# Performance work log

Hardware: AMD Instinct MI355X
Metric: run time of the kernel (lower is better)

Reference implementation:

```python
import jax, jax.numpy as jnp
import numpy as np

M, K, N = 4096, 4096, 4096

def setup_inputs() -> dict:
    key = jax.random.key(0)
    k1, k2, k3 = jax.random.split(key, 3)
    a = jax.random.randint(k1, (M, K), 0, 127, dtype=jnp.int32)
    b = jax.random.randint(k2, (K, N), 0, 127, dtype=jnp.int32)
    scale = jax.random.uniform(k3, (N,), dtype=jnp.float32)
    return {"a": a, "b": b, "scale": scale}

def reference(a, b, scale):
    a8 = a.astype(jnp.int8)
    b8 = b.astype(jnp.int8)
    acc = jnp.matmul(a8, b8, preferred_element_type=jnp.int32)  # [M, N] int32
    # fused per-column (per-output-channel) dequantization scale
    return acc.astype(jnp.float32) * scale[None, :]  # [M, N] float32
```

## Files before the change

### kernel.cpp

```cpp
#include <hip/hip_runtime.h>
#include <stdint.h>

#define M_DIM 4096
#define K_DIM 4096
#define N_DIM 4096

typedef int v4i __attribute__((ext_vector_type(4)));
typedef int int32x4 __attribute__((ext_vector_type(4)));

__device__ __forceinline__ void gload_lds16(const void* g, void* l) {
    __builtin_amdgcn_global_load_lds(
        (const __attribute__((address_space(1))) uint32_t*)g,
        (__attribute__((address_space(3))) uint32_t*)l, 16, 0, 0);
}

__global__ void pack_ab_kernel(const int* __restrict__ a, char* __restrict__ a8,
                               const int* __restrict__ b, char* __restrict__ b8t) {
    __shared__ char tile[64][68];
    if (blockIdx.x < 2048) {
        int idx = blockIdx.x * 256 + threadIdx.x;
        const int stride = 2048 * 256;
        const int total4 = M_DIM * K_DIM / 4;
        for (int i = idx; i < total4; i += stride) {
            int32x4 v = ((const int32x4*)a)[i];
            uint32_t p = (uint32_t)(v.x & 0xff) | ((uint32_t)(v.y & 0xff) << 8) |
                         ((uint32_t)(v.z & 0xff) << 16) | ((uint32_t)(v.w & 0xff) << 24);
            ((uint32_t*)a8)[i] = p;
        }
    } else {
        int bid2 = blockIdx.x - 2048;
        int n0 = (bid2 & 63) * 64;
        int k0 = (bid2 >> 6) * 64;
        int tx = threadIdx.x & 63;
        int ty = threadIdx.x >> 6;
#pragma unroll
        for (int kk = 0; kk < 64; kk += 4) {
            tile[kk + ty][tx] = (char)b[(size_t)(k0 + kk + ty) * N_DIM + n0 + tx];
        }
        __syncthreads();
        int td = threadIdx.x & 15;
        int tn = threadIdx.x >> 4;
#pragma unroll
        for (int nn0 = 0; nn0 < 64; nn0 += 16) {
            int nn = nn0 + tn;
            uint32_t p = (uint32_t)(uint8_t)tile[td * 4 + 0][nn] |
                         ((uint32_t)(uint8_t)tile[td * 4 + 1][nn] << 8) |
                         ((uint32_t)(uint8_t)tile[td * 4 + 2][nn] << 16) |
                         ((uint32_t)(uint8_t)tile[td * 4 + 3][nn] << 24);
            *(uint32_t*)&b8t[(size_t)(n0 + nn) * K_DIM + k0 + td * 4] = p;
        }
    }
}

#define BM 256
#define BN 256
#define BK 128
#define KTILES (K_DIM / BK)

#define BAR __builtin_amdgcn_s_barrier()
#define WAIT_VM4 asm volatile("s_waitcnt vmcnt(4)" ::: "memory")
#define WAIT_VM0 asm volatile("s_waitcnt vmcnt(0)" ::: "memory")

#define DS_A(dst, kk, ib)                                                               \
    _Pragma("unroll") for (int i_ = 0; i_ < 4; ++i_) dst[i_] =                          \
        *(const v4i*)(lds + bufOff + (kk) * 16384 + aOff + ((ib) + i_) * 1024);

#define DS_B(dst, kk)                                                                   \
    _Pragma("unroll") for (int j_ = 0; j_ < 4; ++j_) dst[j_] =                          \
        *(const v4i*)(lds + bufOff + (kk) * 16384 + bOff + j_ * 1024);

#define MM(ib, AF, BF)                                                                  \
    __builtin_amdgcn_s_setprio(1);                                                      \
    _Pragma("unroll") for (int i_ = 0; i_ < 4; ++i_)                                    \
    _Pragma("unroll") for (int j_ = 0; j_ < 4; ++j_)                                    \
        acc[(ib) + i_][j_] =                                                            \
            __builtin_amdgcn_mfma_i32_16x16x64_i8(AF[i_], BF[j_], acc[(ib) + i_][j_],   \
                                                  0, 0, 0);                             \
    __builtin_amdgcn_s_setprio(0);

__global__ __launch_bounds__(512, 2) void gemm_i8_slip(const char* __restrict__ A8,
                                                       const char* __restrict__ B8T,
                                                       const float* __restrict__ scale,
                                                       float* __restrict__ out) {
    __shared__ char lds[131072];

    int tid = threadIdx.x;
    int wave = tid >> 6;
    int lane = tid & 63;
    int wr = wave >> 2;
    int wc = wave & 3;
    int l15 = lane & 15;

    int bid = blockIdx.x;
    int swz = (bid & 7) * 32 + (bid >> 3);
    int bm = swz >> 4;
    int bn = swz & 15;

    int rA = tid >> 2;
    int cc = ((tid & 3) ^ ((tid >> 3) & 3)) << 4;
    const char* aSrc = A8 + (size_t)(bm * BM + rA) * K_DIM + cc;
    const char* bSrc = B8T + (size_t)(bn * BN + rA) * K_DIM + cc;

    int slot = (((lane >> 4) ^ ((lane >> 1) & 3)) << 4);
    int aOff = wr * 8192 + l15 * 64 + slot;
    int bOff = 32768 + wc * 4096 + l15 * 64 + slot;

    v4i acc[8][4];
#pragma unroll
    for (int i = 0; i < 8; ++i)
#pragma unroll
        for (int j = 0; j < 4; ++j) acc[i][j] = (v4i){0, 0, 0, 0};

    auto stage = [&](const char* srcBase, int kt1, int kk, int dstOff) {
        const char* s = srcBase + (size_t)kt1 * BK + kk * 64;
        char* d = (char*)lds + dstOff + wave * 1024;
        gload_lds16(s, d);
        gload_lds16(s + (size_t)128 * K_DIM, d + 8192);
    };

    stage(aSrc, 0, 0, 0);
    stage(bSrc, 0, 0, 32768);
    stage(aSrc, 0, 1, 16384);
    stage(bSrc, 0, 1, 49152);
    WAIT_VM4;
    BAR;

    int bufOff = 0;
    v4i a03[4], a47[4], b0[4];

    for (int kt = 0; kt < KTILES - 1; ++kt) {
        int nbufOff = bufOff ^ 65536;
        stage(aSrc, kt + 1, 0, nbufOff + 0);
        stage(bSrc, kt + 1, 0, nbufOff + 32768);
        DS_A(a03, 0, 0);
        DS_B(b0, 0);
        DS_A(a47, 0, 4);
        MM(0, a03, b0);
        MM(4, a47, b0);
        WAIT_VM4;
        BAR;
        stage(aSrc, kt + 1, 1, nbufOff + 16384);
        stage(bSrc, kt + 1, 1, nbufOff + 49152);
        DS_A(a03, 1, 0);
        DS_B(b0, 1);
        DS_A(a47, 1, 4);
        MM(0, a03, b0);
        MM(4, a47, b0);
        WAIT_VM4;
        BAR;
        bufOff = nbufOff;
    }

    DS_A(a03, 0, 0);
    DS_B(b0, 0);
    DS_A(a47, 0, 4);
    MM(0, a03, b0);
    MM(4, a47, b0);
    WAIT_VM0;
    BAR;
    DS_A(a03, 1, 0);
    DS_B(b0, 1);
    DS_A(a47, 1, 4);
    MM(0, a03, b0);
    MM(4, a47, b0);

    size_t orow0 = (size_t)bm * BM + wr * 128 + (lane >> 4) * 4;
    int ocol0 = bn * BN + wc * 64 + l15;
#pragma unroll
    for (int j = 0; j < 4; ++j) {
        int col = ocol0 + j * 16;
        float s = scale[col];
#pragma unroll
        for (int i = 0; i < 8; ++i) {
            size_t row = orow0 + (size_t)i * 16;
#pragma unroll
            for (int r = 0; r < 4; ++r) {
                out[(row + r) * N_DIM + col] = (float)acc[i][j][r] * s;
            }
        }
    }
}

#define FBM 128
#define FBN 128
#define FBK 64

__global__ __launch_bounds__(256) void gemm_i8_fused_kernel(const int* __restrict__ a,
                                                            const int* __restrict__ b,
                                                            const float* __restrict__ scale,
                                                            float* __restrict__ out) {
    __shared__ char As[FBM * FBK];
    __shared__ char Bs[FBN * FBK];

    int tid = threadIdx.x;
    int wave = tid >> 6;
    int lane = tid & 63;

    int nwg = gridDim.x;
    int cpx = nwg >> 3;
    int bid = blockIdx.x;
    int swz = (bid & 7) * cpx + (bid >> 3);
    int bm = swz >> 5;
    int bn = swz & 31;

    int f0 = tid * 16;
    int m0 = f0 >> 6;
    int k0 = f0 & 63;

    int nn = tid & 127;
    int kh = tid >> 7;

    int wr = wave >> 1;
    int wc = wave & 1;
    int lrow = lane & 15;
    int kgrp = (lane >> 4) * 16;

    v4i acc[4][4];
#pragma unroll
    for (int i = 0; i < 4; ++i)
#pragma unroll
        for (int j = 0; j < 4; ++j) acc[i][j] = (v4i){0, 0, 0, 0};

    const int kTiles = K_DIM / FBK;
    for (int kt = 0; kt < kTiles; ++kt) {
        __syncthreads();
#pragma unroll
        for (int r = 0; r < 2; ++r) {
            const int* src = a + (size_t)(bm * FBM + m0 + r * 64) * K_DIM + kt * FBK + k0;
            uint32_t pk[4];
#pragma unroll
            for (int q = 0; q < 4; ++q) {
                int32x4 v = *(const int32x4*)(src + q * 4);
                pk[q] = (uint32_t)(v.x & 0xff) | ((uint32_t)(v.y & 0xff) << 8) |
                        ((uint32_t)(v.z & 0xff) << 16) | ((uint32_t)(v.w & 0xff) << 24);
            }
            *(v4i*)&As[f0 + r * 4096] = (v4i){(int)pk[0], (int)pk[1], (int)pk[2], (int)pk[3]};
        }
#pragma unroll
        for (int d = 0; d < 8; ++d) {
            uint32_t p = 0;
#pragma unroll
            for (int i = 0; i < 4; ++i) {
                int kk = kt * FBK + kh * 32 + d * 4 + i;
                p |= (uint32_t)(b[(size_t)kk * N_DIM + bn * FBN + nn] & 0xff) << (8 * i);
            }
            *(uint32_t*)&Bs[nn * 64 + kh * 32 + d * 4] = p;
        }
        __syncthreads();

        v4i aF[4], bF[4];
#pragma unroll
        for (int i = 0; i < 4; ++i)
            aF[i] = *(const v4i*)&As[(wr * 64 + i * 16 + lrow) * FBK + kgrp];
#pragma unroll
        for (int j = 0; j < 4; ++j)
            bF[j] = *(const v4i*)&Bs[(wc * 64 + j * 16 + lrow) * FBK + kgrp];
#pragma unroll
        for (int i = 0; i < 4; ++i)
#pragma unroll
            for (int j = 0; j < 4; ++j)
                acc[i][j] = __builtin_amdgcn_mfma_i32_16x16x64_i8(aF[i], bF[j], acc[i][j], 0, 0, 0);
    }

    size_t orow0 = (size_t)bm * FBM + wr * 64;
    int ocol0 = bn * FBN + wc * 64;
#pragma unroll
    for (int j = 0; j < 4; ++j) {
        int col = ocol0 + j * 16 + lrow;
        float s = scale[col];
#pragma unroll
        for (int i = 0; i < 4; ++i) {
            size_t row = orow0 + i * 16 + (lane >> 4) * 4;
#pragma unroll
            for (int r = 0; r < 4; ++r) {
                out[(row + r) * N_DIM + col] = (float)acc[i][j][r] * s;
            }
        }
    }
}

extern "C" void kernel_launch(void* const* d_in, const int* in_sizes, int n_in,
                              void* d_out, int out_size, void* d_ws, size_t ws_size,
                              hipStream_t stream) {
    const int* a = (const int*)d_in[0];
    const int* b = (const int*)d_in[1];
    const float* scale = (const float*)d_in[2];
    float* out = (float*)d_out;

    size_t need = (size_t)M_DIM * K_DIM + (size_t)K_DIM * N_DIM;
    if (ws_size >= need) {
        char* a8 = (char*)d_ws;
        char* b8t = a8 + (size_t)M_DIM * K_DIM;
        pack_ab_kernel<<<2048 + 4096, 256, 0, stream>>>(a, a8, b, b8t);
        gemm_i8_slip<<<256, 512, 0, stream>>>(a8, b8t, scale, out);
    } else {
        gemm_i8_fused_kernel<<<1024, 256, 0, stream>>>(a, b, scale, out);
    }
}
```

Baseline: 97.44 us.

## Deepen GEMM LDS prefetch pipeline to three half-tile stages in flight

Restructures the K-loop so each half-tile's global-to-LDS load is issued one half-tile earlier, reusing the just-consumed half of the current buffer for tile kt+2. This keeps more global loads in flight (wait on vmcnt(8) instead of vmcnt(4)) to hide memory latency behind MFMA work. It adds a peeled epilogue for the last two tiles and relies on barrier ordering to avoid overwriting LDS that is still being read.

New measurement: 94.29 us. 1.03x faster.

```diff
diff --git a/kernel.cpp b/kernel.cpp
--- a/kernel.cpp
+++ b/kernel.cpp
@@ -58,16 +58,17 @@
 #define KTILES (K_DIM / BK)
 
 #define BAR __builtin_amdgcn_s_barrier()
+#define WAIT_VM8 asm volatile("s_waitcnt vmcnt(8)" ::: "memory")
 #define WAIT_VM4 asm volatile("s_waitcnt vmcnt(4)" ::: "memory")
 #define WAIT_VM0 asm volatile("s_waitcnt vmcnt(0)" ::: "memory")
 
-#define DS_A(dst, kk, ib)                                                               \
+#define DS_A(dst, bo, kk, ib)                                                           \
     _Pragma("unroll") for (int i_ = 0; i_ < 4; ++i_) dst[i_] =                          \
-        *(const v4i*)(lds + bufOff + (kk) * 16384 + aOff + ((ib) + i_) * 1024);
-
-#define DS_B(dst, kk)                                                                   \
+        *(const v4i*)(lds + (bo) + (kk) * 16384 + aOff + ((ib) + i_) * 1024);
+
+#define DS_B(dst, bo, kk)                                                               \
     _Pragma("unroll") for (int j_ = 0; j_ < 4; ++j_) dst[j_] =                          \
-        *(const v4i*)(lds + bufOff + (kk) * 16384 + bOff + j_ * 1024);
+        *(const v4i*)(lds + (bo) + (kk) * 16384 + bOff + j_ * 1024);
 
 #define MM(ib, AF, BF)                                                                  \
     __builtin_amdgcn_s_setprio(1);                                                      \
@@ -78,7 +79,7 @@
                                                   0, 0, 0);                             \
     __builtin_amdgcn_s_setprio(0);
 
-__global__ __launch_bounds__(512, 2) void gemm_i8_slip(const char* __restrict__ A8,
+__global__ __launch_bounds__(512, 2) void gemm_i8_deep(const char* __restrict__ A8,
                                                        const char* __restrict__ B8T,
                                                        const float* __restrict__ scale,
                                                        float* __restrict__ out) {
@@ -122,47 +123,68 @@
     stage(bSrc, 0, 0, 32768);
     stage(aSrc, 0, 1, 16384);
     stage(bSrc, 0, 1, 49152);
-    WAIT_VM4;
+    stage(aSrc, 1, 0, 65536 + 0);
+    stage(bSrc, 1, 0, 65536 + 32768);
+    WAIT_VM8;
     BAR;
 
-    int bufOff = 0;
     v4i a03[4], a47[4], b0[4];
 
-    for (int kt = 0; kt < KTILES - 1; ++kt) {
-        int nbufOff = bufOff ^ 65536;
-        stage(aSrc, kt + 1, 0, nbufOff + 0);
-        stage(bSrc, kt + 1, 0, nbufOff + 32768);
-        DS_A(a03, 0, 0);
-        DS_B(b0, 0);
-        DS_A(a47, 0, 4);
+    for (int kt = 0; kt < KTILES - 2; ++kt) {
+        int curBuf = (kt & 1) << 16;
+        int nxtBuf = curBuf ^ 65536;
+        stage(aSrc, kt + 1, 1, nxtBuf + 16384);
+        stage(bSrc, kt + 1, 1, nxtBuf + 49152);
+        DS_A(a03, curBuf, 0, 0);
+        DS_B(b0, curBuf, 0);
+        DS_A(a47, curBuf, 0, 4);
+        MM(0, a03, b0);
+        MM(4, a47, b0);
+        WAIT_VM8;
+        BAR;
+        stage(aSrc, kt + 2, 0, curBuf + 0);
+        stage(bSrc, kt + 2, 0, curBuf + 32768);
+        DS_A(a03, curBuf, 1, 0);
+        DS_B(b0, curBuf, 1);
+        DS_A(a47, curBuf, 1, 4);
+        MM(0, a03, b0);
+        MM(4, a47, b0);
+        WAIT_VM8;
+        BAR;
+    }
+
+    {
+        const int curBuf = ((KTILES - 2) & 1) << 16;
+        const int nxtBuf = curBuf ^ 65536;
+        stage(aSrc, KTILES - 1, 1, nxtBuf + 16384);
+        stage(bSrc, KTILES - 1, 1, nxtBuf + 49152);
+        DS_A(a03, curBuf, 0, 0);
+        DS_B(b0, curBuf, 0);
+        DS_A(a47, curBuf, 0, 4);
+        MM(0, a03, b0);
+        MM(4, a47, b0);
+        WAIT_VM8;
+        BAR;
+        DS_A(a03, curBuf, 1, 0);
+        DS_B(b0, curBuf, 1);
+        DS_A(a47, curBuf, 1, 4);
         MM(0, a03, b0);
         MM(4, a47, b0);
         WAIT_VM4;
         BAR;
-        stage(aSrc, kt + 1, 1, nbufOff + 16384);
-        stage(bSrc, kt + 1, 1, nbufOff + 49152);
-        DS_A(a03, 1, 0);
-        DS_B(b0, 1);
-        DS_A(a47, 1, 4);
-        MM(0, a03, b0);
-        MM(4, a47, b0);
-        WAIT_VM4;
-        BAR;
-        bufOff = nbufOff;
-    }
-
-    DS_A(a03, 0, 0);
-    DS_B(b0, 0);
-    DS_A(a47, 0, 4);
-    MM(0, a03, b0);
-    MM(4, a47, b0);
-    WAIT_VM0;
-    BAR;
-    DS_A(a03, 1, 0);
-    DS_B(b0, 1);
-    DS_A(a47, 1, 4);
-    MM(0, a03, b0);
-    MM(4, a47, b0);
+        DS_A(a03, nxtBuf, 0, 0);
+        DS_B(b0, nxtBuf, 0);
+        DS_A(a47, nxtBuf, 0, 4);
+        MM(0, a03, b0);
+        MM(4, a47, b0);
+        WAIT_VM0;
+        BAR;
+        DS_A(a03, nxtBuf, 1, 0);
+        DS_B(b0, nxtBuf, 1);
+        DS_A(a47, nxtBuf, 1, 4);
+        MM(0, a03, b0);
+        MM(4, a47, b0);
+    }
 
     size_t orow0 = (size_t)bm * BM + wr * 128 + (lane >> 4) * 4;
     int ocol0 = bn * BN + wc * 64 + l15;
@@ -292,7 +314,7 @@
         char* a8 = (char*)d_ws;
         char* b8t = a8 + (size_t)M_DIM * K_DIM;
         pack_ab_kernel<<<2048 + 4096, 256, 0, stream>>>(a, a8, b, b8t);
-        gemm_i8_slip<<<256, 512, 0, stream>>>(a8, b8t, scale, out);
+        gemm_i8_deep<<<256, 512, 0, stream>>>(a8, b8t, scale, out);
     } else {
         gemm_i8_fused_kernel<<<1024, 256, 0, stream>>>(a, b, scale, out);
     }
```

## Replace 256x256 int8 GEMM with smaller 128x128 tiles and higher occupancy

Applied to the files above, without the earlier changes.

Swaps the large-tile GEMM (256x256x128, 512 threads, 128KB LDS, 2 waves/SIMD pairs) for a 128x128x64 tile kernel with 256 threads, 32KB LDS and 4 blocks per CU, launched over 1024 blocks. The pipeline becomes a simple two-deep double buffer with one MFMA group per k-step. The goal is to rely on thread-level parallelism to hide latency instead of the intra-wave software pipeline. In exchange, reuse per loaded byte is halved, so global and LDS traffic per MFMA rise.

Result: slower. 120.1 us (+23.3%).

```diff
diff --git a/kernel.cpp b/kernel.cpp
--- a/kernel.cpp
+++ b/kernel.cpp
@@ -52,49 +52,40 @@
     }
 }
 
-#define BM 256
-#define BN 256
-#define BK 128
+#define BM 128
+#define BN 128
+#define BK 64
 #define KTILES (K_DIM / BK)
 
 #define BAR __builtin_amdgcn_s_barrier()
 #define WAIT_VM4 asm volatile("s_waitcnt vmcnt(4)" ::: "memory")
 #define WAIT_VM0 asm volatile("s_waitcnt vmcnt(0)" ::: "memory")
 
-#define DS_A(dst, kk, ib)                                                               \
-    _Pragma("unroll") for (int i_ = 0; i_ < 4; ++i_) dst[i_] =                          \
-        *(const v4i*)(lds + bufOff + (kk) * 16384 + aOff + ((ib) + i_) * 1024);
-
-#define DS_B(dst, kk)                                                                   \
-    _Pragma("unroll") for (int j_ = 0; j_ < 4; ++j_) dst[j_] =                          \
-        *(const v4i*)(lds + bufOff + (kk) * 16384 + bOff + j_ * 1024);
-
-#define MM(ib, AF, BF)                                                                  \
+#define MM16(AF, BF)                                                                    \
     __builtin_amdgcn_s_setprio(1);                                                      \
     _Pragma("unroll") for (int i_ = 0; i_ < 4; ++i_)                                    \
     _Pragma("unroll") for (int j_ = 0; j_ < 4; ++j_)                                    \
-        acc[(ib) + i_][j_] =                                                            \
-            __builtin_amdgcn_mfma_i32_16x16x64_i8(AF[i_], BF[j_], acc[(ib) + i_][j_],   \
-                                                  0, 0, 0);                             \
+        acc[i_][j_] =                                                                   \
+            __builtin_amdgcn_mfma_i32_16x16x64_i8(AF[i_], BF[j_], acc[i_][j_], 0, 0, 0);\
     __builtin_amdgcn_s_setprio(0);
 
-__global__ __launch_bounds__(512, 2) void gemm_i8_slip(const char* __restrict__ A8,
-                                                       const char* __restrict__ B8T,
-                                                       const float* __restrict__ scale,
-                                                       float* __restrict__ out) {
-    __shared__ char lds[131072];
+__global__ __launch_bounds__(256, 4) void gemm_i8_tlp(const char* __restrict__ A8,
+                                                      const char* __restrict__ B8T,
+                                                      const float* __restrict__ scale,
+                                                      float* __restrict__ out) {
+    __shared__ char lds[32768];
 
     int tid = threadIdx.x;
     int wave = tid >> 6;
     int lane = tid & 63;
-    int wr = wave >> 2;
-    int wc = wave & 3;
+    int wr = wave >> 1;
+    int wc = wave & 1;
     int l15 = lane & 15;
 
     int bid = blockIdx.x;
-    int swz = (bid & 7) * 32 + (bid >> 3);
-    int bm = swz >> 4;
-    int bn = swz & 15;
+    int swz = (bid & 7) * 128 + (bid >> 3);
+    int bm = swz >> 5;
+    int bn = swz & 31;
 
     int rA = tid >> 2;
     int cc = ((tid & 3) ^ ((tid >> 3) & 3)) << 4;
@@ -102,76 +93,71 @@
     const char* bSrc = B8T + (size_t)(bn * BN + rA) * K_DIM + cc;
 
     int slot = (((lane >> 4) ^ ((lane >> 1) & 3)) << 4);
-    int aOff = wr * 8192 + l15 * 64 + slot;
-    int bOff = 32768 + wc * 4096 + l15 * 64 + slot;
-
-    v4i acc[8][4];
-#pragma unroll
-    for (int i = 0; i < 8; ++i)
+    int aOff = wr * 4096 + l15 * 64 + slot;
+    int bOff = 8192 + wc * 4096 + l15 * 64 + slot;
+
+    v4i acc[4][4];
+#pragma unroll
+    for (int i = 0; i < 4; ++i)
 #pragma unroll
         for (int j = 0; j < 4; ++j) acc[i][j] = (v4i){0, 0, 0, 0};
 
-    auto stage = [&](const char* srcBase, int kt1, int kk, int dstOff) {
-        const char* s = srcBase + (size_t)kt1 * BK + kk * 64;
-        char* d = (char*)lds + dstOff + wave * 1024;
-        gload_lds16(s, d);
-        gload_lds16(s + (size_t)128 * K_DIM, d + 8192);
+    auto stage = [&](int kt, int bo) {
+        const char* sa = aSrc + (size_t)kt * BK;
+        const char* sb = bSrc + (size_t)kt * BK;
+        char* da = (char*)lds + bo + wave * 1024;
+        char* db = da + 8192;
+        gload_lds16(sa, da);
+        gload_lds16(sa + (size_t)64 * K_DIM, da + 4096);
+        gload_lds16(sb, db);
+        gload_lds16(sb + (size_t)64 * K_DIM, db + 4096);
     };
 
-    stage(aSrc, 0, 0, 0);
-    stage(bSrc, 0, 0, 32768);
-    stage(aSrc, 0, 1, 16384);
-    stage(bSrc, 0, 1, 49152);
+    stage(0, 0);
+    stage(1, 16384);
     WAIT_VM4;
     BAR;
 
-    int bufOff = 0;
-    v4i a03[4], a47[4], b0[4];
-
-    for (int kt = 0; kt < KTILES - 1; ++kt) {
-        int nbufOff = bufOff ^ 65536;
-        stage(aSrc, kt + 1, 0, nbufOff + 0);
-        stage(bSrc, kt + 1, 0, nbufOff + 32768);
-        DS_A(a03, 0, 0);
-        DS_B(b0, 0);
-        DS_A(a47, 0, 4);
-        MM(0, a03, b0);
-        MM(4, a47, b0);
+    v4i aF[4], bF[4];
+
+    for (int kt = 0; kt < KTILES - 2; ++kt) {
+        int cur = (kt & 1) << 14;
+#pragma unroll
+        for (int i = 0; i < 4; ++i) aF[i] = *(const v4i*)(lds + cur + aOff + i * 1024);
+#pragma unroll
+        for (int j = 0; j < 4; ++j) bF[j] = *(const v4i*)(lds + cur + bOff + j * 1024);
+        MM16(aF, bF);
+        BAR;
+        stage(kt + 2, cur);
         WAIT_VM4;
         BAR;
-        stage(aSrc, kt + 1, 1, nbufOff + 16384);
-        stage(bSrc, kt + 1, 1, nbufOff + 49152);
-        DS_A(a03, 1, 0);
-        DS_B(b0, 1);
-        DS_A(a47, 1, 4);
-        MM(0, a03, b0);
-        MM(4, a47, b0);
-        WAIT_VM4;
+    }
+
+    {
+        int cur = ((KTILES - 2) & 1) << 14;
+#pragma unroll
+        for (int i = 0; i < 4; ++i) aF[i] = *(const v4i*)(lds + cur + aOff + i * 1024);
+#pragma unroll
+        for (int j = 0; j < 4; ++j) bF[j] = *(const v4i*)(lds + cur + bOff + j * 1024);
+        MM16(aF, bF);
+        WAIT_VM0;
         BAR;
-        bufOff = nbufOff;
-    }
-
-    DS_A(a03, 0, 0);
-    DS_B(b0, 0);
-    DS_A(a47, 0, 4);
-    MM(0, a03, b0);
-    MM(4, a47, b0);
-    WAIT_VM0;
-    BAR;
-    DS_A(a03, 1, 0);
-    DS_B(b0, 1);
-    DS_A(a47, 1, 4);
-    MM(0, a03, b0);
-    MM(4, a47, b0);
-
-    size_t orow0 = (size_t)bm * BM + wr * 128 + (lane >> 4) * 4;
+        cur ^= 16384;
+#pragma unroll
+        for (int i = 0; i < 4; ++i) aF[i] = *(const v4i*)(lds + cur + aOff + i * 1024);
+#pragma unroll
+        for (int j = 0; j < 4; ++j) bF[j] = *(const v4i*)(lds + cur + bOff + j * 1024);
+        MM16(aF, bF);
+    }
+
+    size_t orow0 = (size_t)bm * BM + wr * 64 + (lane >> 4) * 4;
     int ocol0 = bn * BN + wc * 64 + l15;
 #pragma unroll
     for (int j = 0; j < 4; ++j) {
         int col = ocol0 + j * 16;
         float s = scale[col];
 #pragma unroll
-        for (int i = 0; i < 8; ++i) {
+        for (int i = 0; i < 4; ++i) {
             size_t row = orow0 + (size_t)i * 16;
 #pragma unroll
             for (int r = 0; r < 4; ++r) {
@@ -292,7 +278,7 @@
         char* a8 = (char*)d_ws;
         char* b8t = a8 + (size_t)M_DIM * K_DIM;
         pack_ab_kernel<<<2048 + 4096, 256, 0, stream>>>(a, a8, b, b8t);
-        gemm_i8_slip<<<256, 512, 0, stream>>>(a8, b8t, scale, out);
+        gemm_i8_tlp<<<1024, 256, 0, stream>>>(a8, b8t, scale, out);
     } else {
         gemm_i8_fused_kernel<<<1024, 256, 0, stream>>>(a, b, scale, out);
     }
```
